# Kernel tuning notes

Measured on AMD Instinct MI355X. Metric: run time of the kernel, lower is better.

## Reference

```python
import jax, jax.numpy as jnp
import numpy as np

B, L, F, H = 8, 1024, 1024, 16
D = F // H  # feat_head = 64
EPS = 1e-5


def setup_inputs() -> dict:
    key = jax.random.key(0)
    ks = jax.random.split(key, 12)
    s = 1.0 / np.sqrt(F)
    inp = {
        "q": jax.random.normal(ks[0], (B, L, F), jnp.float32),
        "k": jax.random.normal(ks[1], (B, L, F), jnp.float32),
        "v": jax.random.normal(ks[2], (B, L, F), jnp.float32),
        "Wq": jax.random.uniform(ks[3], (F, F), jnp.float32, -s, s),
        "bq": jax.random.uniform(ks[4], (F,), jnp.float32, -s, s),
        "Wk": jax.random.uniform(ks[5], (F, F), jnp.float32, -s, s),
        "bk": jax.random.uniform(ks[6], (F,), jnp.float32, -s, s),
        "Wv": jax.random.uniform(ks[7], (F, F), jnp.float32, -s, s),
        "bv": jax.random.uniform(ks[8], (F,), jnp.float32, -s, s),
        "Wf": jax.random.uniform(ks[9], (F, F), jnp.float32, -s, s),
        "bf": jax.random.uniform(ks[10], (F,), jnp.float32, -s, s),
        "gamma": jnp.ones((F,), jnp.float32),
        "beta": jnp.zeros((F,), jnp.float32),
    }
    return inp


def _split_heads(x):
    # (B, L, F) -> (B*H, L, D), matching reshape->transpose(1,2)->reshape
    return x.reshape(B, L, H, D).transpose(0, 2, 1, 3).reshape(B * H, L, D)


def reference(q, k, v, Wq, bq, Wk, bk, Wv, bv, Wf, bf, gamma, beta):
    residual = q
    qh = _split_heads(q @ Wq.T + bq)
    kh = _split_heads(k @ Wk.T + bk)
    vh = _split_heads(v @ Wv.T + bv)
    # scores: (B*H, L, L)
    scores = jnp.einsum('nqd,nkd->nqk', qh, kh) / np.sqrt(D)
    raw_att = jax.nn.softmax(scores, axis=-1)
    att = jnp.einsum('nqk,nkd->nqd', raw_att, vh)  # (B*H, L, D)
    # faithful to original output recombine: reshape(H, B, L, D).permute(1,2,0,3)
    att = att.reshape(H, B, L, D).transpose(1, 2, 0, 3).reshape(B, L, F)
    att = att @ Wf.T + bf
    # dropout in eval mode = identity; activation is None
    x = att + residual
    mu = jnp.mean(x, axis=-1, keepdims=True)
    var = jnp.mean(jnp.square(x - mu), axis=-1, keepdims=True)
    out = (x - mu) * jax.lax.rsqrt(var + EPS) * gamma + beta
    return out, raw_att
```

## Files before the change

### kernel.cpp

```cpp
#include <hip/hip_runtime.h>

#define BB 8
#define LL 1024
#define FF 1024
#define HH 16
#define DD 64
#define NBH 128

typedef __attribute__((ext_vector_type(8))) short bf16x8;
typedef __attribute__((ext_vector_type(4))) float f32x4;

#define GLD_LDS16(g, l)                                                        \
  __builtin_amdgcn_global_load_lds(                                            \
      (const __attribute__((address_space(1))) unsigned int*)(g),              \
      (__attribute__((address_space(3))) unsigned int*)(l), 16, 0, 0)

__device__ __forceinline__ unsigned short f2bf(float f) {
  unsigned int u = __float_as_uint(f);
  unsigned int r = u + 0x7fffu + ((u >> 16) & 1u);
  return (unsigned short)(r >> 16);
}

__global__ __launch_bounds__(256) void cvt3_kernel(const float* __restrict__ s0,
                                                   const float* __restrict__ s1,
                                                   const float* __restrict__ s2,
                                                   short* __restrict__ dst, int n4) {
  int z = blockIdx.y;
  const float* src = (z == 0) ? s0 : (z == 1) ? s1 : s2;
  int i = blockIdx.x * 256 + threadIdx.x;
  if (i >= n4) return;
  float4 v = ((const float4*)src)[i];
  short4 o;
  o.x = (short)f2bf(v.x); o.y = (short)f2bf(v.y);
  o.z = (short)f2bf(v.z); o.w = (short)f2bf(v.w);
  ((short4*)(dst + (size_t)z * n4 * 4))[i] = o;
}

__global__ __launch_bounds__(256) void cvt4_kernel(const float* __restrict__ s0,
                                                   const float* __restrict__ s1,
                                                   const float* __restrict__ s2,
                                                   const float* __restrict__ s3,
                                                   short* __restrict__ dst, int n4) {
  int z = blockIdx.y;
  const float* src = (z == 0) ? s0 : (z == 1) ? s1 : (z == 2) ? s2 : s3;
  int i = blockIdx.x * 256 + threadIdx.x;
  if (i >= n4) return;
  float4 v = ((const float4*)src)[i];
  short4 o;
  o.x = (short)f2bf(v.x); o.y = (short)f2bf(v.y);
  o.z = (short)f2bf(v.z); o.w = (short)f2bf(v.w);
  ((short4*)(dst + (size_t)z * n4 * 4))[i] = o;
}

__global__ __launch_bounds__(256) void proj_qkv(
    const short* __restrict__ Aall, const short* __restrict__ Wall,
    const float* __restrict__ bq, const float* __restrict__ bk,
    const float* __restrict__ bv, short* __restrict__ Dall) {
  const int o = blockIdx.x + (blockIdx.y << 6) + (blockIdx.z << 9);
  const int n = ((o & 7) * 192) + (o >> 3);
  const int z = n >> 9;
  const int r = n & 511;
  const int by = r & 7, bx = r >> 3;

  const short* A  = Aall + (size_t)z * (BB * LL * FF);
  const short* Bt = Wall + (size_t)z * (FF * FF);
  const float* bias = (z == 0) ? bq : (z == 1) ? bk : bv;
  short* dst = Dall + (size_t)z * ((size_t)NBH * LL * DD);
  const float scale = (z == 0) ? 0.125f * 1.44269504088896f : 1.0f;

  __shared__ __attribute__((aligned(16))) short LB[128 * 136];
  short* As = LB;
  short* Bs = LB + 128 * 64;

  const int tid = threadIdx.x;
  const int lane = tid & 63, w = tid >> 6;
  const int wr = w >> 1, wc = w & 1;
  const int row16 = lane & 15, kg = lane >> 4;
  const int m0 = bx * 128, n0 = by * 128;

  const f32x4 z4 = {0.f, 0.f, 0.f, 0.f};
  f32x4 acc[4][4];
  for (int i = 0; i < 4; ++i)
    for (int j = 0; j < 4; ++j) acc[i][j] = z4;

  for (int k0 = 0; k0 < FF; k0 += 64) {
#pragma unroll
    for (int rr = 0; rr < 4; ++rr) {
      int e8 = tid + rr * 256;
      int row = e8 >> 3, cs = ((e8 & 7) ^ (row & 7)) * 8;
      GLD_LDS16(A + (size_t)(m0 + row) * FF + k0 + cs, As + e8 * 8);
      GLD_LDS16(Bt + (size_t)(n0 + row) * FF + k0 + cs, Bs + e8 * 8);
    }
    __syncthreads();
#pragma unroll
    for (int kk2 = 0; kk2 < 2; ++kk2) {
      bf16x8 af[4], bfr[4];
#pragma unroll
      for (int i = 0; i < 4; ++i) {
        int ra = wr * 64 + i * 16 + row16;
        int rb = wc * 64 + i * 16 + row16;
        af[i]  = *(const bf16x8*)(As + ra * 64 + ((((kk2 << 2) | kg) ^ (ra & 7)) << 3));
        bfr[i] = *(const bf16x8*)(Bs + rb * 64 + ((((kk2 << 2) | kg) ^ (rb & 7)) << 3));
      }
#pragma unroll
      for (int i = 0; i < 4; ++i)
#pragma unroll
        for (int j = 0; j < 4; ++j)
          acc[i][j] = __builtin_amdgcn_mfma_f32_16x16x32_bf16(af[i], bfr[j], acc[i][j], 0, 0, 0);
    }
    __syncthreads();
  }

  const int z2 = (z == 2);
#pragma unroll
  for (int i = 0; i < 4; ++i) {
#pragma unroll
    for (int j = 0; j < 4; ++j) {
      int nl = wc * 64 + j * 16 + row16;
      float bn = bias[n0 + nl];
#pragma unroll
      for (int rr = 0; rr < 4; ++rr) {
        int ml = wr * 64 + i * 16 + kg * 4 + rr;
        float val = (acc[i][j][rr] + bn) * scale;
        int rrow = z2 ? nl : ml, ccol = z2 ? ml : nl;
        LB[rrow * 136 + ccol] = (short)f2bf(val);
      }
    }
  }
  __syncthreads();
  const int b = m0 >> 10;
  const int lbase = m0 & 1023;
#pragma unroll
  for (int rr = 0; rr < 8; ++rr) {
    int e = tid + rr * 256;
    int row = e >> 4, c8 = e & 15;
    uint4 val = *(const uint4*)(LB + row * 136 + c8 * 8);
    if (!z2) {
      int l = lbase + row;
      int h = (n0 + c8 * 8) >> 6, d = (c8 & 7) * 8;
      *(uint4*)(dst + (((size_t)(b * HH + h)) * LL + l) * DD + d) = val;
    } else {
      int h = (n0 + row) >> 6, d = (n0 + row) & 63;
      int l = lbase + c8 * 8;
      *(uint4*)(dst + (((size_t)(b * HH + h)) * DD + d) * LL + l) = val;
    }
  }
}

__global__ __launch_bounds__(256) void attn_kernel(
    const short* __restrict__ Qh, const short* __restrict__ Kh,
    const short* __restrict__ Vt, float* __restrict__ Patt,
    short* __restrict__ attb) {
  const int o = blockIdx.x + (blockIdx.y << 4);
  const int n = ((o & 7) << 8) + (o >> 3);
  const int bh = n >> 4;
  const int q0 = (n & 15) * 64;
  const int tid = threadIdx.x;
  const int lane = tid & 63, w = tid >> 6;
  const int row16 = lane & 15, kg = lane >> 4;

  __shared__ __attribute__((aligned(16))) short Qs[64 * 64];
  __shared__ __attribute__((aligned(16))) short Ks[2][64 * 64];
  __shared__ __attribute__((aligned(16))) short Vts[2][64 * 64];
  __shared__ __attribute__((aligned(16))) short PsT[4][16 * 64];

  auto kbuf3 = [&](int i) -> short* {
    return (i == 2) ? &Vts[0][0] : &Ks[i][0];
  };

#define STAGE_K(tt, dstp)                                                      \
  {                                                                            \
    int e8a = tid, rowa = e8a >> 3, c8a = (e8a & 7) ^ (rowa & 7);              \
    GLD_LDS16(Kh + ((size_t)bh * LL + (tt) * 64 + rowa) * DD + c8a * 8,        \
              (dstp) + e8a * 8);                                               \
    int e8b = tid + 256, rowb = e8b >> 3, c8b = (e8b & 7) ^ (rowb & 7);        \
    GLD_LDS16(Kh + ((size_t)bh * LL + (tt) * 64 + rowb) * DD + c8b * 8,        \
              (dstp) + e8b * 8);                                               \
  }
#define STAGE_V(tt, dstp)                                                      \
  {                                                                            \
    int e8a = tid, rowa = e8a >> 3, c8a = (e8a & 7) ^ (rowa & 7);              \
    GLD_LDS16(Vt + ((size_t)bh * DD + rowa) * LL + (tt) * 64 + c8a * 8,        \
              (dstp) + e8a * 8);                                               \
    int e8b = tid + 256, rowb = e8b >> 3, c8b = (e8b & 7) ^ (rowb & 7);        \
    GLD_LDS16(Vt + ((size_t)bh * DD + rowb) * LL + (tt) * 64 + c8b * 8,        \
              (dstp) + e8b * 8);                                               \
  }

  {
    int e8a = tid, rowa = e8a >> 3, c8a = (e8a & 7) ^ (rowa & 7);
    GLD_LDS16(Qh + ((size_t)bh * LL + q0 + rowa) * DD + c8a * 8, Qs + e8a * 8);
    int e8b = tid + 256, rowb = e8b >> 3, c8b = (e8b & 7) ^ (rowb & 7);
    GLD_LDS16(Qh + ((size_t)bh * LL + q0 + rowb) * DD + c8b * 8, Qs + e8b * 8);
  }
  STAGE_K(0, kbuf3(0));
  STAGE_K(1, kbuf3(1));
  asm volatile("s_waitcnt vmcnt(2)" ::: "memory");
  __builtin_amdgcn_s_barrier();

  const int qrow = w * 16 + row16;
  bf16x8 aq0 = *(const bf16x8*)(Qs + qrow * 64 + ((kg ^ (qrow & 7)) << 3));
  bf16x8 aq1 = *(const bf16x8*)(Qs + qrow * 64 + (((kg + 4) ^ (qrow & 7)) << 3));

  const f32x4 z4 = {0.f, 0.f, 0.f, 0.f};
  float lsum = 0.f;

  for (int t = 0; t < 16; ++t) {
    const short* kb = kbuf3(t % 3);
    if (t < 14) {
      short* kd = kbuf3((t + 2) % 3);
      STAGE_K(t + 2, kd);
    }
    f32x4 s[4] = {z4, z4, z4, z4};
    __builtin_amdgcn_s_setprio(1);
#pragma unroll
    for (int tt = 0; tt < 4; ++tt) {
      int krow = tt * 16 + row16;
      bf16x8 b0 = *(const bf16x8*)(kb + krow * 64 + ((kg ^ (krow & 7)) << 3));
      bf16x8 b1 = *(const bf16x8*)(kb + krow * 64 + (((kg + 4) ^ (krow & 7)) << 3));
      s[tt] = __builtin_amdgcn_mfma_f32_16x16x32_bf16(b0, aq0, s[tt], 0, 0, 0);
      s[tt] = __builtin_amdgcn_mfma_f32_16x16x32_bf16(b1, aq1, s[tt], 0, 0, 0);
    }
    __builtin_amdgcn_s_setprio(0);
#pragma unroll
    for (int tt = 0; tt < 4; ++tt)
#pragma unroll
      for (int rr = 0; rr < 4; ++rr) lsum += exp2f(s[tt][rr]);
    if (t < 14) {
      asm volatile("s_waitcnt vmcnt(2)" ::: "memory");
    } else {
      asm volatile("s_waitcnt vmcnt(0)" ::: "memory");
    }
    __builtin_amdgcn_s_barrier();
  }
  lsum += __shfl_xor(lsum, 16);
  lsum += __shfl_xor(lsum, 32);
  const float lc = __log2f(lsum);

  f32x4 oT[4] = {z4, z4, z4, z4};

  STAGE_K(0, &Ks[0][0]);
  STAGE_V(0, &Vts[0][0]);
  asm volatile("s_waitcnt vmcnt(0)" ::: "memory");
  __builtin_amdgcn_s_barrier();
  for (int t = 0; t < 16; ++t) {
    const int cur = t & 1;
    if (t < 15) {
      STAGE_K(t + 1, &Ks[cur ^ 1][0]);
      STAGE_V(t + 1, &Vts[cur ^ 1][0]);
    }
    f32x4 s[4] = {z4, z4, z4, z4};
    __builtin_amdgcn_s_setprio(1);
#pragma unroll
    for (int tt = 0; tt < 4; ++tt) {
      int krow = tt * 16 + row16;
      bf16x8 b0 = *(const bf16x8*)(&Ks[cur][krow * 64 + ((kg ^ (krow & 7)) << 3)]);
      bf16x8 b1 = *(const bf16x8*)(&Ks[cur][krow * 64 + (((kg + 4) ^ (krow & 7)) << 3)]);
      s[tt] = __builtin_amdgcn_mfma_f32_16x16x32_bf16(b0, aq0, s[tt], 0, 0, 0);
      s[tt] = __builtin_amdgcn_mfma_f32_16x16x32_bf16(b1, aq1, s[tt], 0, 0, 0);
    }
    __builtin_amdgcn_s_setprio(0);
    const int qq = q0 + w * 16 + row16;
    const int k0 = t * 64;
#pragma unroll
    for (int tt = 0; tt < 4; ++tt) {
      f32x4 pv;
#pragma unroll
      for (int rr = 0; rr < 4; ++rr) pv[rr] = exp2f(s[tt][rr] - lc);
      __builtin_nontemporal_store(
          pv, (f32x4*)(Patt + ((size_t)bh * LL + qq) * LL + k0 + tt * 16 + kg * 4));
      short4 ps;
      ps.x = (short)f2bf(pv[0]); ps.y = (short)f2bf(pv[1]);
      ps.z = (short)f2bf(pv[2]); ps.w = (short)f2bf(pv[3]);
      int c = ((tt * 2 + (kg >> 1)) ^ (row16 & 7));
      *(short4*)(&PsT[w][row16 * 64 + c * 8 + (kg & 1) * 4]) = ps;
    }
    bf16x8 pb0 = *(const bf16x8*)(&PsT[w][row16 * 64 + ((kg ^ (row16 & 7)) << 3)]);
    bf16x8 pb1 = *(const bf16x8*)(&PsT[w][row16 * 64 + (((4 + kg) ^ (row16 & 7)) << 3)]);
    __builtin_amdgcn_s_setprio(1);
#pragma unroll
    for (int td = 0; td < 4; ++td) {
      int trow = td * 16 + row16;
      bf16x8 v0 = *(const bf16x8*)(&Vts[cur][trow * 64 + ((kg ^ (trow & 7)) << 3)]);
      bf16x8 v1 = *(const bf16x8*)(&Vts[cur][trow * 64 + (((kg + 4) ^ (trow & 7)) << 3)]);
      oT[td] = __builtin_amdgcn_mfma_f32_16x16x32_bf16(v0, pb0, oT[td], 0, 0, 0);
      oT[td] = __builtin_amdgcn_mfma_f32_16x16x32_bf16(v1, pb1, oT[td], 0, 0, 0);
    }
    __builtin_amdgcn_s_setprio(0);
    if (t < 15) {
      asm volatile("s_waitcnt vmcnt(4)" ::: "memory");
      __builtin_amdgcn_s_barrier();
    }
  }

  const int iblk = bh >> 3;
  const int jb = bh & 7;
  const int qq = q0 + w * 16 + row16;
#pragma unroll
  for (int td = 0; td < 4; ++td) {
    short4 ov;
    ov.x = (short)f2bf(oT[td][0]); ov.y = (short)f2bf(oT[td][1]);
    ov.z = (short)f2bf(oT[td][2]); ov.w = (short)f2bf(oT[td][3]);
    *(short4*)(attb + ((size_t)jb * LL + qq) * FF + iblk * 64 + td * 16 + kg * 4) = ov;
  }
#undef STAGE_K
#undef STAGE_V
}

__global__ __launch_bounds__(256) void proj_out(
    const short* __restrict__ A, const short* __restrict__ Bt,
    const float* __restrict__ bias, const float* __restrict__ resid,
    float* __restrict__ xb) {
  const int o = blockIdx.x + (blockIdx.y << 6);
  const int n = ((o & 7) << 6) + (o >> 3);
  const int by = n & 7, bx = n >> 3;

  __shared__ __attribute__((aligned(16))) short As[128 * 64];
  __shared__ __attribute__((aligned(16))) short Bs[128 * 64];

  const int tid = threadIdx.x;
  const int lane = tid & 63, w = tid >> 6;
  const int wr = w >> 1, wc = w & 1;
  const int row16 = lane & 15, kg = lane >> 4;
  const int m0 = bx * 128, n0 = by * 128;

  const f32x4 z4 = {0.f, 0.f, 0.f, 0.f};
  f32x4 acc[4][4];
  for (int i = 0; i < 4; ++i)
    for (int j = 0; j < 4; ++j) acc[i][j] = z4;

  for (int k0 = 0; k0 < FF; k0 += 64) {
#pragma unroll
    for (int rr = 0; rr < 4; ++rr) {
      int e8 = tid + rr * 256;
      int row = e8 >> 3, cs = ((e8 & 7) ^ (row & 7)) * 8;
      GLD_LDS16(A + (size_t)(m0 + row) * FF + k0 + cs, As + e8 * 8);
      GLD_LDS16(Bt + (size_t)(n0 + row) * FF + k0 + cs, Bs + e8 * 8);
    }
    __syncthreads();
#pragma unroll
    for (int kk2 = 0; kk2 < 2; ++kk2) {
      bf16x8 af[4], bfr[4];
#pragma unroll
      for (int i = 0; i < 4; ++i) {
        int ra = wr * 64 + i * 16 + row16;
        int rb = wc * 64 + i * 16 + row16;
        af[i]  = *(const bf16x8*)(As + ra * 64 + ((((kk2 << 2) | kg) ^ (ra & 7)) << 3));
        bfr[i] = *(const bf16x8*)(Bs + rb * 64 + ((((kk2 << 2) | kg) ^ (rb & 7)) << 3));
      }
#pragma unroll
      for (int i = 0; i < 4; ++i)
#pragma unroll
        for (int j = 0; j < 4; ++j)
          acc[i][j] = __builtin_amdgcn_mfma_f32_16x16x32_bf16(af[i], bfr[j], acc[i][j], 0, 0, 0);
    }
    __syncthreads();
  }

#pragma unroll
  for (int i = 0; i < 4; ++i) {
#pragma unroll
    for (int j = 0; j < 4; ++j) {
      int ncol = n0 + wc * 64 + j * 16 + row16;
      float bn = bias[ncol];
#pragma unroll
      for (int rr = 0; rr < 4; ++rr) {
        int m = m0 + wr * 64 + i * 16 + kg * 4 + rr;
        xb[(size_t)m * FF + ncol] = acc[i][j][rr] + bn + resid[(size_t)m * FF + ncol];
      }
    }
  }
}

__global__ __launch_bounds__(256) void ln_kernel(const float* __restrict__ xb,
                                                 const float* __restrict__ gamma,
                                                 const float* __restrict__ beta,
                                                 float* __restrict__ out) {
  const int row = blockIdx.x;
  const int tid = threadIdx.x;
  const float4 v = *(const float4*)(xb + (size_t)row * FF + tid * 4);
  float s = v.x + v.y + v.z + v.w;
  float s2 = v.x * v.x + v.y * v.y + v.z * v.z + v.w * v.w;
#pragma unroll
  for (int o = 1; o < 64; o <<= 1) {
    s += __shfl_xor(s, o);
    s2 += __shfl_xor(s2, o);
  }
  __shared__ float ss[4], ss2[4];
  int w = tid >> 6, lane = tid & 63;
  if (lane == 0) { ss[w] = s; ss2[w] = s2; }
  __syncthreads();
  s = ss[0] + ss[1] + ss[2] + ss[3];
  s2 = ss2[0] + ss2[1] + ss2[2] + ss2[3];
  float mu = s * (1.0f / 1024.0f);
  float var = s2 * (1.0f / 1024.0f) - mu * mu;
  float rs = rsqrtf(var + 1e-5f);
  float4 g = *(const float4*)(gamma + tid * 4);
  float4 be = *(const float4*)(beta + tid * 4);
  float4 o;
  o.x = (v.x - mu) * rs * g.x + be.x;
  o.y = (v.y - mu) * rs * g.y + be.y;
  o.z = (v.z - mu) * rs * g.z + be.z;
  o.w = (v.w - mu) * rs * g.w + be.w;
  *(float4*)(out + (size_t)row * FF + tid * 4) = o;
}

extern "C" void kernel_launch(void* const* d_in, const int* in_sizes, int n_in,
                              void* d_out, int out_size, void* d_ws, size_t ws_size,
                              hipStream_t stream) {
  const float* q  = (const float*)d_in[0];
  const float* k  = (const float*)d_in[1];
  const float* v  = (const float*)d_in[2];
  const float* Wq = (const float*)d_in[3];
  const float* bq = (const float*)d_in[4];
  const float* Wk = (const float*)d_in[5];
  const float* bk = (const float*)d_in[6];
  const float* Wv = (const float*)d_in[7];
  const float* bv = (const float*)d_in[8];
  const float* Wf = (const float*)d_in[9];
  const float* bf = (const float*)d_in[10];
  const float* gamma = (const float*)d_in[11];
  const float* beta  = (const float*)d_in[12];

  float* out = (float*)d_out;
  float* Patt = out + (size_t)BB * LL * FF;

  char* ws = (char*)d_ws;
  const size_t MB = (size_t)1 << 20;
  short* qb = (short*)(ws + 0 * MB);
  short* Wb = (short*)(ws + 48 * MB);
  short* Qh = (short*)(ws + 56 * MB);
  short* Kh = (short*)(ws + 72 * MB);
  short* Vt = (short*)(ws + 88 * MB);
  short* attb = qb;
  float* xb = (float*)(ws + 16 * MB);

  const int nAct4 = BB * LL * FF / 4;
  const int nW4 = FF * FF / 4;
  cvt3_kernel<<<dim3((nAct4 + 255) / 256, 3), 256, 0, stream>>>(q, k, v, qb, nAct4);
  cvt4_kernel<<<dim3((nW4 + 255) / 256, 4), 256, 0, stream>>>(Wq, Wk, Wv, Wf, Wb, nW4);

  proj_qkv<<<dim3(64, 8, 3), 256, 0, stream>>>(qb, Wb, bq, bk, bv, Qh);
  attn_kernel<<<dim3(16, 128), 256, 0, stream>>>(Qh, Kh, Vt, Patt, attb);
  proj_out<<<dim3(64, 8), 256, 0, stream>>>(attb, Wb + 3 * (size_t)FF * FF, bf, q, xb);
  ln_kernel<<<8192, 256, 0, stream>>>(xb, gamma, beta, out);
}
```

Baseline: 291.7 us.

## Fuse two-pass attention into single pass with deferred normalization

Replaces the two-pass softmax (first pass computing row sums, second recomputing QK^T for probabilities and PV) with a single pass that accumulates unnormalized exp and PV. Probabilities are kept in registers as bf16 and scaled by the inverse row sum at the end. K and V staging becomes a three-deep ring buffer. This halves the QK^T MFMA work and K loads, but holds 128 packed registers per thread, raising register pressure and possibly spilling. The stored attention probabilities now carry bf16 rounding rather than fp32 precision.

After: 405.3 us. 1.39x slower.

```diff
diff --git a/kernel.cpp b/kernel.cpp
--- a/kernel.cpp
+++ b/kernel.cpp
@@ -160,13 +160,9 @@
   const int row16 = lane & 15, kg = lane >> 4;
 
   __shared__ __attribute__((aligned(16))) short Qs[64 * 64];
-  __shared__ __attribute__((aligned(16))) short Ks[2][64 * 64];
-  __shared__ __attribute__((aligned(16))) short Vts[2][64 * 64];
+  __shared__ __attribute__((aligned(16))) short Ks[3][64 * 64];
+  __shared__ __attribute__((aligned(16))) short Vts[3][64 * 64];
   __shared__ __attribute__((aligned(16))) short PsT[4][16 * 64];
-
-  auto kbuf3 = [&](int i) -> short* {
-    return (i == 2) ? &Vts[0][0] : &Ks[i][0];
-  };
 
 #define STAGE_K(tt, dstp)                                                      \
   {                                                                            \
@@ -193,9 +189,11 @@
     int e8b = tid + 256, rowb = e8b >> 3, c8b = (e8b & 7) ^ (rowb & 7);
     GLD_LDS16(Qh + ((size_t)bh * LL + q0 + rowb) * DD + c8b * 8, Qs + e8b * 8);
   }
-  STAGE_K(0, kbuf3(0));
-  STAGE_K(1, kbuf3(1));
-  asm volatile("s_waitcnt vmcnt(2)" ::: "memory");
+  STAGE_K(0, &Ks[0][0]);
+  STAGE_V(0, &Vts[0][0]);
+  STAGE_K(1, &Ks[1][0]);
+  STAGE_V(1, &Vts[1][0]);
+  asm volatile("s_waitcnt vmcnt(4)" ::: "memory");
   __builtin_amdgcn_s_barrier();
 
   const int qrow = w * 16 + row16;
@@ -204,50 +202,16 @@
 
   const f32x4 z4 = {0.f, 0.f, 0.f, 0.f};
   float lsum = 0.f;
-
+  f32x4 oT[4] = {z4, z4, z4, z4};
+  uint2 pk[16][4];
+
+#pragma unroll
   for (int t = 0; t < 16; ++t) {
-    const short* kb = kbuf3(t % 3);
+    const int cur = t % 3;
     if (t < 14) {
-      short* kd = kbuf3((t + 2) % 3);
-      STAGE_K(t + 2, kd);
-    }
-    f32x4 s[4] = {z4, z4, z4, z4};
-    __builtin_amdgcn_s_setprio(1);
-#pragma unroll
-    for (int tt = 0; tt < 4; ++tt) {
-      int krow = tt * 16 + row16;
-      bf16x8 b0 = *(const bf16x8*)(kb + krow * 64 + ((kg ^ (krow & 7)) << 3));
-      bf16x8 b1 = *(const bf16x8*)(kb + krow * 64 + (((kg + 4) ^ (krow & 7)) << 3));
-      s[tt] = __builtin_amdgcn_mfma_f32_16x16x32_bf16(b0, aq0, s[tt], 0, 0, 0);
-      s[tt] = __builtin_amdgcn_mfma_f32_16x16x32_bf16(b1, aq1, s[tt], 0, 0, 0);
-    }
-    __builtin_amdgcn_s_setprio(0);
-#pragma unroll
-    for (int tt = 0; tt < 4; ++tt)
-#pragma unroll
-      for (int rr = 0; rr < 4; ++rr) lsum += exp2f(s[tt][rr]);
-    if (t < 14) {
-      asm volatile("s_waitcnt vmcnt(2)" ::: "memory");
-    } else {
-      asm volatile("s_waitcnt vmcnt(0)" ::: "memory");
-    }
-    __builtin_amdgcn_s_barrier();
-  }
-  lsum += __shfl_xor(lsum, 16);
-  lsum += __shfl_xor(lsum, 32);
-  const float lc = __log2f(lsum);
-
-  f32x4 oT[4] = {z4, z4, z4, z4};
-
-  STAGE_K(0, &Ks[0][0]);
-  STAGE_V(0, &Vts[0][0]);
-  asm volatile("s_waitcnt vmcnt(0)" ::: "memory");
-  __builtin_amdgcn_s_barrier();
-  for (int t = 0; t < 16; ++t) {
-    const int cur = t & 1;
-    if (t < 15) {
-      STAGE_K(t + 1, &Ks[cur ^ 1][0]);
-      STAGE_V(t + 1, &Vts[cur ^ 1][0]);
+      const int nxt = (t + 2) % 3;
+      STAGE_K(t + 2, &Ks[nxt][0]);
+      STAGE_V(t + 2, &Vts[nxt][0]);
     }
     f32x4 s[4] = {z4, z4, z4, z4};
     __builtin_amdgcn_s_setprio(1);
@@ -260,18 +224,18 @@
       s[tt] = __builtin_amdgcn_mfma_f32_16x16x32_bf16(b1, aq1, s[tt], 0, 0, 0);
     }
     __builtin_amdgcn_s_setprio(0);
-    const int qq = q0 + w * 16 + row16;
-    const int k0 = t * 64;
 #pragma unroll
     for (int tt = 0; tt < 4; ++tt) {
-      f32x4 pv;
-#pragma unroll
-      for (int rr = 0; rr < 4; ++rr) pv[rr] = exp2f(s[tt][rr] - lc);
-      __builtin_nontemporal_store(
-          pv, (f32x4*)(Patt + ((size_t)bh * LL + qq) * LL + k0 + tt * 16 + kg * 4));
+      f32x4 pu;
+#pragma unroll
+      for (int rr = 0; rr < 4; ++rr) {
+        pu[rr] = exp2f(s[tt][rr]);
+        lsum += pu[rr];
+      }
       short4 ps;
-      ps.x = (short)f2bf(pv[0]); ps.y = (short)f2bf(pv[1]);
-      ps.z = (short)f2bf(pv[2]); ps.w = (short)f2bf(pv[3]);
+      ps.x = (short)f2bf(pu[0]); ps.y = (short)f2bf(pu[1]);
+      ps.z = (short)f2bf(pu[2]); ps.w = (short)f2bf(pu[3]);
+      pk[t][tt] = *(uint2*)&ps;
       int c = ((tt * 2 + (kg >> 1)) ^ (row16 & 7));
       *(short4*)(&PsT[w][row16 * 64 + c * 8 + (kg & 1) * 4]) = ps;
     }
@@ -287,20 +251,43 @@
       oT[td] = __builtin_amdgcn_mfma_f32_16x16x32_bf16(v1, pb1, oT[td], 0, 0, 0);
     }
     __builtin_amdgcn_s_setprio(0);
-    if (t < 15) {
+    if (t < 14) {
       asm volatile("s_waitcnt vmcnt(4)" ::: "memory");
       __builtin_amdgcn_s_barrier();
+    } else if (t == 14) {
+      asm volatile("s_waitcnt vmcnt(0)" ::: "memory");
+      __builtin_amdgcn_s_barrier();
+    }
+  }
+
+  lsum += __shfl_xor(lsum, 16);
+  lsum += __shfl_xor(lsum, 32);
+  const float linv = 1.0f / lsum;
+
+  const int qq = q0 + w * 16 + row16;
+  float* prow = Patt + ((size_t)bh * LL + qq) * LL;
+#pragma unroll
+  for (int t = 0; t < 16; ++t) {
+#pragma unroll
+    for (int tt = 0; tt < 4; ++tt) {
+      uint2 u = pk[t][tt];
+      f32x4 pv;
+      pv[0] = __uint_as_float(u.x << 16) * linv;
+      pv[1] = __uint_as_float(u.x & 0xffff0000u) * linv;
+      pv[2] = __uint_as_float(u.y << 16) * linv;
+      pv[3] = __uint_as_float(u.y & 0xffff0000u) * linv;
+      __builtin_nontemporal_store(
+          pv, (f32x4*)(prow + t * 64 + tt * 16 + kg * 4));
     }
   }
 
   const int iblk = bh >> 3;
   const int jb = bh & 7;
-  const int qq = q0 + w * 16 + row16;
 #pragma unroll
   for (int td = 0; td < 4; ++td) {
     short4 ov;
-    ov.x = (short)f2bf(oT[td][0]); ov.y = (short)f2bf(oT[td][1]);
-    ov.z = (short)f2bf(oT[td][2]); ov.w = (short)f2bf(oT[td][3]);
+    ov.x = (short)f2bf(oT[td][0] * linv); ov.y = (short)f2bf(oT[td][1] * linv);
+    ov.z = (short)f2bf(oT[td][2] * linv); ov.w = (short)f2bf(oT[td][3] * linv);
     *(short4*)(attb + ((size_t)jb * LL + qq) * FF + iblk * 64 + td * 16 + kg * 4) = ov;
   }
 #undef STAGE_K
```
